# Kernel optimization log

Measured on AMD Instinct MI355X. Metric: run time of the kernel, lower is better.

The kernel has to match this reference:

```python
import jax, jax.numpy as jnp
import numpy as np

jax.config.update("jax_enable_x64", True)  # faithful int64 fixed-point requantize

B, K, N = 2048, 4096, 8192
INT32_MAX_MINUS = 2147418112  # threshold from multiply_by_quantize_mul


def setup_inputs() -> dict:
    key = jax.random.key(0)
    k1, k2, k3 = jax.random.split(key, 3)
    x = jax.random.randint(k1, (B, K), -128, 128, dtype=jnp.int8)
    weights = jax.random.randint(k2, (N, K), -128, 128, dtype=jnp.int8)
    bias = jax.random.randint(k3, (N, 1), -1024, 1024, dtype=jnp.int32)
    return {
        "x": x,
        "weights": weights,
        "bias": bias,
        "q_mantissa": 1431655765,   # ~2/3 in Q31 fixed point
        "exponent": -3,
        "output_zero_point": -5,
    }


def multiply_by_quantize_mul(x, q_mantissa, exponent):
    # Python precedence in original: (q_mantissa + (1<<15)) >> 16
    reduced_mantissa = ((q_mantissa + (1 << 15)) >> 16) if q_mantissa < INT32_MAX_MINUS else 32767
    total_shifts = 15 - exponent
    x = x * np.int64(reduced_mantissa)
    x = x + np.int64(1 << (total_shifts - 1))  # rounding term
    return jnp.right_shift(x, total_shifts)    # arithmetic shift on signed int64


def reference(x, weights, bias, q_mantissa, exponent, output_zero_point):
    # int8 GEMM accumulated in int32: result[b, n] = sum_k x[b, k] * w[n, k]
    acc = jnp.einsum("bk,nk->bn", x.astype(jnp.int32), weights.astype(jnp.int32))
    acc = acc + bias.T  # bias [N,1] -> [1,N], broadcast over batch
    acc = multiply_by_quantize_mul(acc.astype(jnp.int64), q_mantissa, exponent)
    acc = acc + np.int64(output_zero_point)
    out = jnp.clip(acc, -128, 127).astype(jnp.int8)
    return out
```

## Files before the change

kernel.cpp:

```cpp
#include <hip/hip_runtime.h>

#define DEVI __device__ __forceinline__

typedef int i32x4 __attribute__((ext_vector_type(4)));

static constexpr int Bdim = 2048;
static constexpr int Kdim = 4096;
static constexpr int Ndim = 8192;
static constexpr int BK   = 128;
static constexpr int NT   = Kdim / BK;

typedef __attribute__((address_space(1))) const unsigned int gas_t;
typedef __attribute__((address_space(3))) unsigned int las_t;

DEVI void gload_lds16(const void* g, void* l) {
    __builtin_amdgcn_global_load_lds((gas_t*)g, (las_t*)l, 16, 0, 0);
}

DEVI int pack4(i32x4 v) {
    return (v[0] & 255) | ((v[1] & 255) << 8) | ((v[2] & 255) << 16) | (v[3] << 24);
}

__global__ void pack_i32_to_i8(const int* __restrict__ in, char* __restrict__ out, int n16) {
    int i = blockIdx.x * blockDim.x + threadIdx.x;
    if (i >= n16) return;
    const i32x4* src = (const i32x4*)in + (size_t)i * 4;
    i32x4 r;
    r[0] = pack4(src[0]);
    r[1] = pack4(src[1]);
    r[2] = pack4(src[2]);
    r[3] = pack4(src[3]);
    ((i32x4*)out)[i] = r;
}

#define CFENCE asm volatile("" ::: "memory")
DEVI void bar() { CFENCE; __builtin_amdgcn_s_barrier(); CFENCE; }
#define WAITVM(N) asm volatile("s_waitcnt vmcnt(" #N ")" ::: "memory")
#define PRIO1 __builtin_amdgcn_s_setprio(1)
#define PRIO0 __builtin_amdgcn_s_setprio(0)

#define QUAD(MB, A, B)                                                           \
    do {                                                                         \
        _Pragma("unroll") for (int mm = 0; mm < 4; ++mm)                         \
        _Pragma("unroll") for (int n = 0; n < 4; ++n)                            \
            acc[(MB) + mm][n] = __builtin_amdgcn_mfma_i32_16x16x64_i8(           \
                (A)[mm], (B)[n], acc[(MB) + mm][n], 0, 0, 0);                    \
    } while (0)

#define PHASE(CUR, KS, STG, VM)                                                  \
    {                                                                            \
        _Pragma("unroll") for (int mm = 0; mm < 8; ++mm) a[mm] = rdA(CUR, KS, mm); \
        _Pragma("unroll") for (int n = 0; n < 4; ++n)    b[n]  = rdB(CUR, KS, n);  \
        STG;                                                                     \
        PRIO1; QUAD(0, a, b); QUAD(4, a + 4, b); PRIO0;                          \
        VM;                                                                      \
        bar();                                                                   \
    }

__attribute__((amdgpu_waves_per_eu(2, 2)))
__global__ __launch_bounds__(512, 2)
void gemm13(const char* __restrict__ A8, const char* __restrict__ B8,
            const int* __restrict__ bias,
            const int* __restrict__ qm_p, const int* __restrict__ ex_p,
            const int* __restrict__ zp_p, int* __restrict__ out) {
    __shared__ i32x4 smem4[8192];
    char* smem = (char*)smem4;

    const int tid  = threadIdx.x;
    const int wid  = tid >> 6;
    const int lane = tid & 63;
    const int l15  = lane & 15;
    const int lks  = lane >> 4;
    const int wr   = wid >> 2;
    const int wc   = wid & 3;

    const int bid = blockIdx.x;
    const int swz = (bid & 7) * 32 + (bid >> 3);
    const int bm  = swz >> 5;
    const int bn  = swz & 31;
    const int arow0 = bm * 256;
    const int brow0 = bn * 256;

    const int swsel = lks ^ ((l15 >> 1) & 3);
    const int a_rd16 = (wr * 128 + l15) * 4 + swsel;
    const int b_rd16 = 4096 + (wc * 64 + l15) * 4 + swsel;

    const int st_c = (tid & 3) ^ ((tid >> 3) & 3);
    const char* agp = A8 + (size_t)(arow0 + (tid >> 2)) * Kdim + st_c * 16;
    const char* bgp = B8 + (size_t)(brow0 + (tid >> 2)) * Kdim + st_c * 16;

    auto stage = [&](int isb, int t, int ks) {
        const char* gp = (isb ? bgp : agp) + (size_t)t * BK + ks * 64;
        const int lb = (isb ? 65536 : 0) + (t & 1) * 32768 + ks * 16384 + tid * 16;
        gload_lds16(gp, &smem[lb]);
        gload_lds16(gp + (size_t)128 * Kdim, &smem[lb + 8192]);
    };
    auto rdA = [&](int buf, int ks, int m) {
        return smem4[buf * 2048 + ks * 1024 + a_rd16 + m * 64];
    };
    auto rdB = [&](int buf, int ks, int n) {
        return smem4[buf * 2048 + ks * 1024 + b_rd16 + n * 64];
    };

    i32x4 acc[8][4] = {};
    i32x4 a[8], b[4];

    stage(0, 0, 0); stage(1, 0, 0);
    stage(0, 0, 1); stage(1, 0, 1);
    stage(0, 1, 0); stage(1, 1, 0);
    WAITVM(4);
    bar();

    int t = 0;
    for (; t < NT - 2; ++t) {
        const int buf = t & 1;
        PHASE(buf, 0, (stage(0, t + 1, 1), stage(1, t + 1, 1)), ((void)0));
        PHASE(buf, 1, (stage(0, t + 2, 0), stage(1, t + 2, 0)), WAITVM(4));
    }
    {
        const int buf = t & 1;
        PHASE(buf, 0, (stage(0, t + 1, 1), stage(1, t + 1, 1)), ((void)0));
        PHASE(buf, 1, ((void)0), WAITVM(0));
    }
    ++t;
    {
        const int buf = t & 1;
        PHASE(buf, 0, ((void)0), ((void)0));
        PHASE(buf, 1, ((void)0), ((void)0));
    }

    const int qm = *qm_p;
    const int ex = *ex_p;
    const int zp = *zp_p;
    const int rm = (qm < 2147418112) ? ((qm + (1 << 15)) >> 16) : 32767;
    const int shifts = 15 - ex;
    const long long rnd = (shifts > 0) ? (1LL << (shifts - 1)) : 0;

    int bv[4];
#pragma unroll
    for (int n = 0; n < 4; ++n) bv[n] = bias[brow0 + wc * 64 + n * 16 + l15];

#pragma unroll
    for (int m = 0; m < 8; ++m) {
        const int row0 = arow0 + wr * 128 + m * 16 + lks * 4;
#pragma unroll
        for (int n = 0; n < 4; ++n) {
            const int col = brow0 + wc * 64 + n * 16 + l15;
#pragma unroll
            for (int j = 0; j < 4; ++j) {
                long long v = (long long)(acc[m][n][j] + bv[n]) * rm + rnd;
                v >>= shifts;
                v += zp;
                v = v < -128 ? -128 : (v > 127 ? 127 : v);
                out[(size_t)(row0 + j) * Ndim + col] = (int)v;
            }
        }
    }
}

extern "C" void kernel_launch(void* const* d_in, const int* in_sizes, int n_in,
                              void* d_out, int out_size, void* d_ws, size_t ws_size,
                              hipStream_t stream) {
    const int* x32  = (const int*)d_in[0];
    const int* w32  = (const int*)d_in[1];
    const int* bias = (const int*)d_in[2];
    const int* qm   = (const int*)d_in[3];
    const int* ex   = (const int*)d_in[4];
    const int* zp   = (const int*)d_in[5];
    int* out = (int*)d_out;

    char* xa = (char*)d_ws;
    char* wa = xa + (size_t)Bdim * Kdim;
    const int nx16 = Bdim * Kdim / 16;
    const int nw16 = Ndim * Kdim / 16;
    pack_i32_to_i8<<<(nx16 + 255) / 256, 256, 0, stream>>>(x32, xa, nx16);
    pack_i32_to_i8<<<(nw16 + 255) / 256, 256, 0, stream>>>(w32, wa, nw16);

    const int grid = (Bdim / 256) * (Ndim / 256);
    gemm13<<<grid, 512, 0, stream>>>(xa, wa, bias, qm, ex, zp, out);
}
```

Before: 102.9 us.

## Switch GEMM to triple-buffered BK=64 pipeline with staggered half-tile LDS reads

Replaces the double-buffered BK=128 split-phase pipeline with a three-slot ring of BK=64 tiles, prefetching two tiles ahead with one barrier per iteration. LDS use drops from 128KB to 96KB. The A fragment loads are split into halves interleaved with MFMA groups, and the order is swapped between wave rows to stagger LDS bank pressure. The aim is better overlap of loads with MFMAs and fewer barriers per unit of compute. The cost is twice as many iterations, and the vmcnt accounting and the t%3 indexing add overhead.

Measured after the change: 106.5 us. 3.5% more time.

```diff
diff --git a/kernel.cpp b/kernel.cpp
--- a/kernel.cpp
+++ b/kernel.cpp
@@ -7,7 +7,7 @@
 static constexpr int Bdim = 2048;
 static constexpr int Kdim = 4096;
 static constexpr int Ndim = 8192;
-static constexpr int BK   = 128;
+static constexpr int BK   = 64;
 static constexpr int NT   = Kdim / BK;
 
 typedef __attribute__((address_space(1))) const unsigned int gas_t;
@@ -36,34 +36,29 @@
 #define CFENCE asm volatile("" ::: "memory")
 DEVI void bar() { CFENCE; __builtin_amdgcn_s_barrier(); CFENCE; }
 #define WAITVM(N) asm volatile("s_waitcnt vmcnt(" #N ")" ::: "memory")
+#define SCHB __builtin_amdgcn_sched_barrier(0)
 #define PRIO1 __builtin_amdgcn_s_setprio(1)
 #define PRIO0 __builtin_amdgcn_s_setprio(0)
 
-#define QUAD(MB, A, B)                                                           \
+#define QUADH(MB)                                                                \
     do {                                                                         \
         _Pragma("unroll") for (int mm = 0; mm < 4; ++mm)                         \
         _Pragma("unroll") for (int n = 0; n < 4; ++n)                            \
             acc[(MB) + mm][n] = __builtin_amdgcn_mfma_i32_16x16x64_i8(           \
-                (A)[mm], (B)[n], acc[(MB) + mm][n], 0, 0, 0);                    \
+                a[(MB) + mm], b[n], acc[(MB) + mm][n], 0, 0, 0);                 \
     } while (0)
 
-#define PHASE(CUR, KS, STG, VM)                                                  \
-    {                                                                            \
-        _Pragma("unroll") for (int mm = 0; mm < 8; ++mm) a[mm] = rdA(CUR, KS, mm); \
-        _Pragma("unroll") for (int n = 0; n < 4; ++n)    b[n]  = rdB(CUR, KS, n);  \
-        STG;                                                                     \
-        PRIO1; QUAD(0, a, b); QUAD(4, a + 4, b); PRIO0;                          \
-        VM;                                                                      \
-        bar();                                                                   \
-    }
+#define LDAH(MB)                                                                 \
+    _Pragma("unroll") for (int mm = 0; mm < 4; ++mm)                             \
+        a[(MB) + mm] = smem4[cb + a_rd16 + ((MB) + mm) * 64]
 
 __attribute__((amdgpu_waves_per_eu(2, 2)))
 __global__ __launch_bounds__(512, 2)
-void gemm13(const char* __restrict__ A8, const char* __restrict__ B8,
+void gemm14(const char* __restrict__ A8, const char* __restrict__ B8,
             const int* __restrict__ bias,
             const int* __restrict__ qm_p, const int* __restrict__ ex_p,
             const int* __restrict__ zp_p, int* __restrict__ out) {
-    __shared__ i32x4 smem4[8192];
+    __shared__ i32x4 smem4[6144];
     char* smem = (char*)smem4;
 
     const int tid  = threadIdx.x;
@@ -83,50 +78,50 @@
 
     const int swsel = lks ^ ((l15 >> 1) & 3);
     const int a_rd16 = (wr * 128 + l15) * 4 + swsel;
-    const int b_rd16 = 4096 + (wc * 64 + l15) * 4 + swsel;
+    const int b_rd16 = 1024 + (wc * 64 + l15) * 4 + swsel;
 
     const int st_c = (tid & 3) ^ ((tid >> 3) & 3);
     const char* agp = A8 + (size_t)(arow0 + (tid >> 2)) * Kdim + st_c * 16;
     const char* bgp = B8 + (size_t)(brow0 + (tid >> 2)) * Kdim + st_c * 16;
 
-    auto stage = [&](int isb, int t, int ks) {
-        const char* gp = (isb ? bgp : agp) + (size_t)t * BK + ks * 64;
-        const int lb = (isb ? 65536 : 0) + (t & 1) * 32768 + ks * 16384 + tid * 16;
-        gload_lds16(gp, &smem[lb]);
-        gload_lds16(gp + (size_t)128 * Kdim, &smem[lb + 8192]);
-    };
-    auto rdA = [&](int buf, int ks, int m) {
-        return smem4[buf * 2048 + ks * 1024 + a_rd16 + m * 64];
-    };
-    auto rdB = [&](int buf, int ks, int n) {
-        return smem4[buf * 2048 + ks * 1024 + b_rd16 + n * 64];
+    auto stage = [&](int t) {
+        const int lb = (t % 3) * 32768 + tid * 16;
+        const size_t ko = (size_t)t * BK;
+        gload_lds16(agp + ko,                      &smem[lb]);
+        gload_lds16(agp + ko + (size_t)128 * Kdim, &smem[lb + 8192]);
+        gload_lds16(bgp + ko,                      &smem[lb + 16384]);
+        gload_lds16(bgp + ko + (size_t)128 * Kdim, &smem[lb + 24576]);
     };
 
     i32x4 acc[8][4] = {};
-    i32x4 a[8], b[4];
 
-    stage(0, 0, 0); stage(1, 0, 0);
-    stage(0, 0, 1); stage(1, 0, 1);
-    stage(0, 1, 0); stage(1, 1, 0);
+    stage(0);
+    stage(1);
     WAITVM(4);
     bar();
 
-    int t = 0;
-    for (; t < NT - 2; ++t) {
-        const int buf = t & 1;
-        PHASE(buf, 0, (stage(0, t + 1, 1), stage(1, t + 1, 1)), ((void)0));
-        PHASE(buf, 1, (stage(0, t + 2, 0), stage(1, t + 2, 0)), WAITVM(4));
-    }
-    {
-        const int buf = t & 1;
-        PHASE(buf, 0, (stage(0, t + 1, 1), stage(1, t + 1, 1)), ((void)0));
-        PHASE(buf, 1, ((void)0), WAITVM(0));
-    }
-    ++t;
-    {
-        const int buf = t & 1;
-        PHASE(buf, 0, ((void)0), ((void)0));
-        PHASE(buf, 1, ((void)0), ((void)0));
+    for (int t = 0; t < NT; ++t) {
+        const int cb = (t % 3) * 2048;
+        if (t + 2 < NT) stage(t + 2);
+        i32x4 a[8], b[4];
+#pragma unroll
+        for (int n = 0; n < 4; ++n) b[n] = smem4[cb + b_rd16 + n * 64];
+        if (wr == 0) {
+            LDAH(0);
+            PRIO1; QUADH(0); PRIO0;
+            SCHB;
+            LDAH(4);
+            PRIO1; QUADH(4); PRIO0;
+        } else {
+            LDAH(4);
+            PRIO1; QUADH(4); PRIO0;
+            SCHB;
+            LDAH(0);
+            PRIO1; QUADH(0); PRIO0;
+        }
+        if (t + 2 < NT) { WAITVM(4); }
+        else            { WAITVM(0); }
+        bar();
     }
 
     const int qm = *qm_p;
@@ -177,5 +172,5 @@
     pack_i32_to_i8<<<(nw16 + 255) / 256, 256, 0, stream>>>(w32, wa, nw16);
 
     const int grid = (Bdim / 256) * (Ndim / 256);
-    gemm13<<<grid, 512, 0, stream>>>(xa, wa, bias, qm, ex, zp, out);
+    gemm14<<<grid, 512, 0, stream>>>(xa, wa, bias, qm, ex, zp, out);
 }
```
